# Performance work log

Measured on AMD Instinct MI355X. Metric: run time of the kernel, lower is better.

Reference implementation:

```python
import jax, jax.numpy as jnp
import numpy as np

QMAX = 127.0  # int8 symmetric

def fake_quant(v):
    # symmetric per-tensor int8 quant -> dequant
    s = jnp.maximum(jnp.max(jnp.abs(v)), 1e-8) / QMAX
    return jnp.round(jnp.clip(v / s, -QMAX, QMAX)) * s

def setup_inputs() -> dict:
    key = jax.random.key(0)
    k1, k2, k3 = jax.random.split(key, 3)
    B, C, H, W = 64, 3, 224, 224
    D, P = 768, 8
    x = jax.random.normal(k1, (B, C, H, W), dtype=jnp.float32)
    w = jax.random.normal(k2, (D, C, P, P), dtype=jnp.float32) * 0.02
    b = jax.random.normal(k3, (D,), dtype=jnp.float32) * 0.02
    return {"x": x, "w": w, "b": b}

def reference(x, w, b):
    B, C, H, W = x.shape
    D, _, P, _ = w.shape
    gh, gw = H // P, W // P
    # quantized conv (HMQConv2d): fake-quant activations and weights, then patchify GEMM
    xq = fake_quant(x)
    wq = fake_quant(w)
    # extract non-overlapping PxP patches: [B, C, gh, P, gw, P]
    xp = xq.reshape(B, C, gh, P, gw, P)
    # conv stride=kernel=P  ==  patch matmul: out [B, gh, gw, D]
    out = jnp.einsum('bchpwq,dchq->bhwd', xp.transpose(0, 1, 2, 3, 4, 5), wq,
                     optimize=True) if False else jnp.einsum('bcxpyq,dcpq->bxyd', xp, wq)
    out = out + b
    # flatten(2).transpose(1,2): [B, N, D]
    out = out.reshape(B, gh * gw, D)
    # norm is Identity (norm_layer=None)
    return out
```

## Files before the change

### kernel.cpp

```cpp
#include <hip/hip_runtime.h>
#include <stdint.h>


typedef short bf16x8 __attribute__((ext_vector_type(8)));
using f32x4 = __attribute__((ext_vector_type(4))) float;

static __device__ __forceinline__ uint16_t f2bfbits(float f) {
  uint32_t u = __float_as_uint(f);
  u += 0x7FFFu + ((u >> 16) & 1u);
  return (uint16_t)(u >> 16);
}

static __device__ __forceinline__ uint32_t q2(float a, float b, float inv_s) {
  float qa = rintf(fminf(fmaxf(a * inv_s, -127.0f), 127.0f));
  float qb = rintf(fminf(fmaxf(b * inv_s, -127.0f), 127.0f));
  return (uint32_t)f2bfbits(qa) | ((uint32_t)f2bfbits(qb) << 16);
}

__global__ void absmax_x1_k(const float4* __restrict__ v, int n,
                            float* __restrict__ partials) {
  __shared__ float red[4];
  float m = 0.0f;
  for (int i = blockIdx.x * blockDim.x + threadIdx.x; i < n;
       i += gridDim.x * blockDim.x) {
    float4 u = v[i];
    m = fmaxf(m, fabsf(u.x)); m = fmaxf(m, fabsf(u.y));
    m = fmaxf(m, fabsf(u.z)); m = fmaxf(m, fabsf(u.w));
  }
#pragma unroll
  for (int off = 32; off > 0; off >>= 1) m = fmaxf(m, __shfl_down(m, off, 64));
  if ((threadIdx.x & 63) == 0) red[threadIdx.x >> 6] = m;
  __syncthreads();
  if (threadIdx.x == 0) {
    m = fmaxf(fmaxf(red[0], red[1]), fmaxf(red[2], red[3]));
    partials[blockIdx.x] = m;
  }
}

__global__ void absmax_x2_k(const float* __restrict__ partials,
                            float* __restrict__ s_out) {
  __shared__ float red[16];
  float m = partials[threadIdx.x];
#pragma unroll
  for (int off = 32; off > 0; off >>= 1) m = fmaxf(m, __shfl_down(m, off, 64));
  if ((threadIdx.x & 63) == 0) red[threadIdx.x >> 6] = m;
  __syncthreads();
  if (threadIdx.x == 0) {
#pragma unroll
    for (int i = 1; i < 16; ++i) m = fmaxf(m, red[i]);
    s_out[0] = fmaxf(m, 1e-8f) * (1.0f / 127.0f);
  }
}

__global__ void absmax_w_k(const float4* __restrict__ v, int n,
                           float* __restrict__ s_out) {
  __shared__ float red[16];
  float m = 0.0f;
  for (int i = threadIdx.x; i < n; i += blockDim.x) {
    float4 u = v[i];
    m = fmaxf(m, fabsf(u.x)); m = fmaxf(m, fabsf(u.y));
    m = fmaxf(m, fabsf(u.z)); m = fmaxf(m, fabsf(u.w));
  }
#pragma unroll
  for (int off = 32; off > 0; off >>= 1) m = fmaxf(m, __shfl_down(m, off, 64));
  if ((threadIdx.x & 63) == 0) red[threadIdx.x >> 6] = m;
  __syncthreads();
  if (threadIdx.x == 0) {
#pragma unroll
    for (int i = 1; i < 16; ++i) m = fmaxf(m, red[i]);
    s_out[0] = fmaxf(m, 1e-8f) * (1.0f / 127.0f);
  }
}

__global__ void quant_w_k(const float4* __restrict__ w, uint2* __restrict__ Wq,
                          const float* __restrict__ slots, int n) {
  int tid = blockIdx.x * blockDim.x + threadIdx.x;
  if (tid >= n) return;
  float inv = 1.0f / slots[1];
  float4 u = w[tid];
  Wq[tid] = make_uint2(q2(u.x, u.y, inv), q2(u.z, u.w, inv));
}

#define BM  128
#define BN  128
#define LDP 72

__global__ __launch_bounds__(256) void gemm_k(
    const float4* __restrict__ x4, const uint16_t* __restrict__ Wq,
    const float* __restrict__ bias, const float* __restrict__ slots,
    float* __restrict__ out) {
  __shared__ uint16_t As[BM * LDP];
  __shared__ uint16_t Ws[BN * LDP];

  const int m0   = blockIdx.y * BM;
  const int n0   = blockIdx.x * BN;
  const int tid  = threadIdx.x;
  const int lane = tid & 63;
  const int wid  = tid >> 6;
  const int wm   = wid >> 1;
  const int wn   = wid & 1;
  const int r0   = tid >> 3;
  const int c8   = tid & 7;
  const int lm   = lane & 15;
  const int lq   = lane >> 4;

  const float sx = slots[0];
  const float sw = slots[1];
  const float inv_sx = 1.0f / sx;

  int xbase[4];
#pragma unroll
  for (int i = 0; i < 4; ++i) {
    int m  = m0 + r0 + i * 32;
    int b  = m / 784;
    int rr = m - b * 784;
    int gx = rr / 28;
    int gy = rr - gx * 28;
    xbase[i] = (b * 672 + gx * 8 + c8) * 56 + gy * 2;
  }

  f32x4 acc[4][4] = {};

  for (int kc = 0; kc < 3; ++kc) {
#pragma unroll
    for (int i = 0; i < 4; ++i) {
      int row = r0 + i * 32;
      float4 a0 = x4[xbase[i] + kc * 12544];
      float4 a1 = x4[xbase[i] + kc * 12544 + 1];
      uint4 q;
      q.x = q2(a0.x, a0.y, inv_sx);
      q.y = q2(a0.z, a0.w, inv_sx);
      q.z = q2(a1.x, a1.y, inv_sx);
      q.w = q2(a1.z, a1.w, inv_sx);
      *(uint4*)(&As[row * LDP + c8 * 8]) = q;
      uint4 vb = *(const uint4*)(Wq + (size_t)(n0 + row) * 192 + kc * 64 + c8 * 8);
      *(uint4*)(&Ws[row * LDP + c8 * 8]) = vb;
    }
    __syncthreads();

#pragma unroll
    for (int kk = 0; kk < 2; ++kk) {
      const int colk = kk * 32 + lq * 8;
      bf16x8 af[4], bfr[4];
#pragma unroll
      for (int t = 0; t < 4; ++t) {
        af[t]  = *(const bf16x8*)(&As[(wm * 64 + t * 16 + lm) * LDP + colk]);
        bfr[t] = *(const bf16x8*)(&Ws[(wn * 64 + t * 16 + lm) * LDP + colk]);
      }
#pragma unroll
      for (int tm = 0; tm < 4; ++tm)
#pragma unroll
        for (int tn = 0; tn < 4; ++tn)
          acc[tm][tn] = __builtin_amdgcn_mfma_f32_16x16x32_bf16(
              af[tm], bfr[tn], acc[tm][tn], 0, 0, 0);
    }
    __syncthreads();
  }

  const float scale = sx * sw;
#pragma unroll
  for (int tn = 0; tn < 4; ++tn) {
    int col = n0 + wn * 64 + tn * 16 + lm;
    float bv = bias[col];
#pragma unroll
    for (int tm = 0; tm < 4; ++tm) {
      int rbase = m0 + wm * 64 + tm * 16 + lq * 4;
#pragma unroll
      for (int r = 0; r < 4; ++r) {
        out[(size_t)(rbase + r) * 768 + col] = acc[tm][tn][r] * scale + bv;
      }
    }
  }
}


extern "C" void kernel_launch(void* const* d_in, const int* in_sizes, int n_in,
                              void* d_out, int out_size, void* d_ws, size_t ws_size,
                              hipStream_t stream) {
  const float4* x = (const float4*)d_in[0];
  const float4* w = (const float4*)d_in[1];
  const float* bias = (const float*)d_in[2];
  float* out = (float*)d_out;

  char* ws = (char*)d_ws;
  float* slots    = (float*)ws;
  float* partials = (float*)(ws + 256);
  uint16_t* Wq    = (uint16_t*)(ws + 8192);

  const int nx4 = 9633792 / 4;
  const int nw4 = 147456 / 4;

  absmax_x1_k<<<1024, 256, 0, stream>>>(x, nx4, partials);
  absmax_x2_k<<<1, 1024, 0, stream>>>(partials, slots + 0);
  absmax_w_k<<<1, 1024, 0, stream>>>(w, nw4, slots + 1);
  quant_w_k<<<144, 256, 0, stream>>>(w, (uint2*)Wq, slots, nw4);
  gemm_k<<<dim3(6, 392), 256, 0, stream>>>(x, Wq, bias, slots, out);
}
```

Before: 243.2 us.

## Drop LDS staging and quantize fragments directly from global in GEMM

Merges the x and w absmax reductions into one launch with a shared finalize kernel, and removes the separate weight-quantization kernel. The GEMM now has each wave load its own MFMA A and B fragments straight from global memory and quantize them in registers. This removes the LDS tiles and `__syncthreads` barriers, and cuts the launch count from five to three. In exchange, A and B fragments are loaded and quantized redundantly across waves, and the weights are re-quantized in every block, which leans on L1/L2 caching.

```diff
diff --git a/kernel.cpp b/kernel.cpp
--- a/kernel.cpp
+++ b/kernel.cpp
@@ -10,22 +10,40 @@
   u += 0x7FFFu + ((u >> 16) & 1u);
   return (uint16_t)(u >> 16);
 }
-
 static __device__ __forceinline__ uint32_t q2(float a, float b, float inv_s) {
   float qa = rintf(fminf(fmaxf(a * inv_s, -127.0f), 127.0f));
   float qb = rintf(fminf(fmaxf(b * inv_s, -127.0f), 127.0f));
   return (uint32_t)f2bfbits(qa) | ((uint32_t)f2bfbits(qb) << 16);
 }
+static __device__ __forceinline__ bf16x8 quant_frag(const float4* p, float inv_s) {
+  float4 a0 = p[0], a1 = p[1];
+  uint4 q;
+  q.x = q2(a0.x, a0.y, inv_s);
+  q.y = q2(a0.z, a0.w, inv_s);
+  q.z = q2(a1.x, a1.y, inv_s);
+  q.w = q2(a1.z, a1.w, inv_s);
+  return __builtin_bit_cast(bf16x8, q);
+}
 
-__global__ void absmax_x1_k(const float4* __restrict__ v, int n,
-                            float* __restrict__ partials) {
+#define NBX 1024
+#define NBW 64
+__global__ void absmax_k(const float4* __restrict__ x, int nx4,
+                         const float4* __restrict__ w, int nw4,
+                         float* __restrict__ partials) {
   __shared__ float red[4];
   float m = 0.0f;
-  for (int i = blockIdx.x * blockDim.x + threadIdx.x; i < n;
-       i += gridDim.x * blockDim.x) {
-    float4 u = v[i];
-    m = fmaxf(m, fabsf(u.x)); m = fmaxf(m, fabsf(u.y));
-    m = fmaxf(m, fabsf(u.z)); m = fmaxf(m, fabsf(u.w));
+  if (blockIdx.x < NBX) {
+    for (int i = blockIdx.x * 256 + threadIdx.x; i < nx4; i += NBX * 256) {
+      float4 u = x[i];
+      m = fmaxf(m, fabsf(u.x)); m = fmaxf(m, fabsf(u.y));
+      m = fmaxf(m, fabsf(u.z)); m = fmaxf(m, fabsf(u.w));
+    }
+  } else {
+    for (int i = (blockIdx.x - NBX) * 256 + threadIdx.x; i < nw4; i += NBW * 256) {
+      float4 u = w[i];
+      m = fmaxf(m, fabsf(u.x)); m = fmaxf(m, fabsf(u.y));
+      m = fmaxf(m, fabsf(u.z)); m = fmaxf(m, fabsf(u.w));
+    }
   }
 #pragma unroll
   for (int off = 32; off > 0; off >>= 1) m = fmaxf(m, __shfl_down(m, off, 64));
@@ -37,124 +55,83 @@
   }
 }
 
-__global__ void absmax_x2_k(const float* __restrict__ partials,
-                            float* __restrict__ s_out) {
+__global__ void finalize_k(const float* __restrict__ partials,
+                           float* __restrict__ slots) {
   __shared__ float red[16];
-  float m = partials[threadIdx.x];
+  int tid = threadIdx.x;
+  float m = partials[tid];
 #pragma unroll
   for (int off = 32; off > 0; off >>= 1) m = fmaxf(m, __shfl_down(m, off, 64));
-  if ((threadIdx.x & 63) == 0) red[threadIdx.x >> 6] = m;
+  if ((tid & 63) == 0) red[tid >> 6] = m;
   __syncthreads();
-  if (threadIdx.x == 0) {
+  if (tid == 0) {
 #pragma unroll
     for (int i = 1; i < 16; ++i) m = fmaxf(m, red[i]);
-    s_out[0] = fmaxf(m, 1e-8f) * (1.0f / 127.0f);
+    slots[0] = fmaxf(m, 1e-8f) * (1.0f / 127.0f);
+  }
+  if (tid >= 64 && tid < 128) {
+    float mw = partials[NBX + (tid - 64)];
+#pragma unroll
+    for (int off = 32; off > 0; off >>= 1) mw = fmaxf(mw, __shfl_down(mw, off, 64));
+    if (tid == 64) slots[1] = fmaxf(mw, 1e-8f) * (1.0f / 127.0f);
   }
 }
 
-__global__ void absmax_w_k(const float4* __restrict__ v, int n,
-                           float* __restrict__ s_out) {
-  __shared__ float red[16];
-  float m = 0.0f;
-  for (int i = threadIdx.x; i < n; i += blockDim.x) {
-    float4 u = v[i];
-    m = fmaxf(m, fabsf(u.x)); m = fmaxf(m, fabsf(u.y));
-    m = fmaxf(m, fabsf(u.z)); m = fmaxf(m, fabsf(u.w));
-  }
-#pragma unroll
-  for (int off = 32; off > 0; off >>= 1) m = fmaxf(m, __shfl_down(m, off, 64));
-  if ((threadIdx.x & 63) == 0) red[threadIdx.x >> 6] = m;
-  __syncthreads();
-  if (threadIdx.x == 0) {
-#pragma unroll
-    for (int i = 1; i < 16; ++i) m = fmaxf(m, red[i]);
-    s_out[0] = fmaxf(m, 1e-8f) * (1.0f / 127.0f);
-  }
-}
-
-__global__ void quant_w_k(const float4* __restrict__ w, uint2* __restrict__ Wq,
-                          const float* __restrict__ slots, int n) {
-  int tid = blockIdx.x * blockDim.x + threadIdx.x;
-  if (tid >= n) return;
-  float inv = 1.0f / slots[1];
-  float4 u = w[tid];
-  Wq[tid] = make_uint2(q2(u.x, u.y, inv), q2(u.z, u.w, inv));
-}
-
-#define BM  128
-#define BN  128
-#define LDP 72
-
 __global__ __launch_bounds__(256) void gemm_k(
-    const float4* __restrict__ x4, const uint16_t* __restrict__ Wq,
+    const float4* __restrict__ x4, const float4* __restrict__ w4,
     const float* __restrict__ bias, const float* __restrict__ slots,
     float* __restrict__ out) {
-  __shared__ uint16_t As[BM * LDP];
-  __shared__ uint16_t Ws[BN * LDP];
-
-  const int m0   = blockIdx.y * BM;
-  const int n0   = blockIdx.x * BN;
   const int tid  = threadIdx.x;
   const int lane = tid & 63;
   const int wid  = tid >> 6;
   const int wm   = wid >> 1;
   const int wn   = wid & 1;
-  const int r0   = tid >> 3;
-  const int c8   = tid & 7;
   const int lm   = lane & 15;
   const int lq   = lane >> 4;
+  const int m0   = blockIdx.y * 128;
+  const int n0   = blockIdx.x * 128;
 
   const float sx = slots[0];
   const float sw = slots[1];
   const float inv_sx = 1.0f / sx;
+  const float inv_sw = 1.0f / sw;
 
-  int xbase[4];
+  int abase[4];
 #pragma unroll
-  for (int i = 0; i < 4; ++i) {
-    int m  = m0 + r0 + i * 32;
+  for (int tm = 0; tm < 4; ++tm) {
+    int m  = m0 + wm * 64 + tm * 16 + lm;
     int b  = m / 784;
     int rr = m - b * 784;
     int gx = rr / 28;
     int gy = rr - gx * 28;
-    xbase[i] = (b * 672 + gx * 8 + c8) * 56 + gy * 2;
+    abase[tm] = (b * 672 + gx * 8) * 56 + gy * 2;
   }
+  int bbase[4];
+#pragma unroll
+  for (int tn = 0; tn < 4; ++tn)
+    bbase[tn] = (n0 + wn * 64 + tn * 16 + lm) * 48;
 
   f32x4 acc[4][4] = {};
 
-  for (int kc = 0; kc < 3; ++kc) {
 #pragma unroll
-    for (int i = 0; i < 4; ++i) {
-      int row = r0 + i * 32;
-      float4 a0 = x4[xbase[i] + kc * 12544];
-      float4 a1 = x4[xbase[i] + kc * 12544 + 1];
-      uint4 q;
-      q.x = q2(a0.x, a0.y, inv_sx);
-      q.y = q2(a0.z, a0.w, inv_sx);
-      q.z = q2(a1.x, a1.y, inv_sx);
-      q.w = q2(a1.z, a1.w, inv_sx);
-      *(uint4*)(&As[row * LDP + c8 * 8]) = q;
-      uint4 vb = *(const uint4*)(Wq + (size_t)(n0 + row) * 192 + kc * 64 + c8 * 8);
-      *(uint4*)(&Ws[row * LDP + c8 * 8]) = vb;
-    }
-    __syncthreads();
-
+  for (int ks = 0; ks < 6; ++ks) {
+    const int c = ks >> 1;
+    const int p = (ks & 1) * 4 + lq;
+    const int aoff = c * 12544 + p * 56;
+    const int boff = ks * 8 + lq * 2;
+    bf16x8 af[4], bf[4];
 #pragma unroll
-    for (int kk = 0; kk < 2; ++kk) {
-      const int colk = kk * 32 + lq * 8;
-      bf16x8 af[4], bfr[4];
+    for (int tm = 0; tm < 4; ++tm)
+      af[tm] = quant_frag(&x4[abase[tm] + aoff], inv_sx);
 #pragma unroll
-      for (int t = 0; t < 4; ++t) {
-        af[t]  = *(const bf16x8*)(&As[(wm * 64 + t * 16 + lm) * LDP + colk]);
-        bfr[t] = *(const bf16x8*)(&Ws[(wn * 64 + t * 16 + lm) * LDP + colk]);
-      }
+    for (int tn = 0; tn < 4; ++tn)
+      bf[tn] = quant_frag(&w4[bbase[tn] + boff], inv_sw);
 #pragma unroll
-      for (int tm = 0; tm < 4; ++tm)
+    for (int tm = 0; tm < 4; ++tm)
 #pragma unroll
-        for (int tn = 0; tn < 4; ++tn)
-          acc[tm][tn] = __builtin_amdgcn_mfma_f32_16x16x32_bf16(
-              af[tm], bfr[tn], acc[tm][tn], 0, 0, 0);
-    }
-    __syncthreads();
+      for (int tn = 0; tn < 4; ++tn)
+        acc[tm][tn] = __builtin_amdgcn_mfma_f32_16x16x32_bf16(
+            af[tm], bf[tn], acc[tm][tn], 0, 0, 0);
   }
 
   const float scale = sx * sw;
@@ -166,9 +143,8 @@
     for (int tm = 0; tm < 4; ++tm) {
       int rbase = m0 + wm * 64 + tm * 16 + lq * 4;
 #pragma unroll
-      for (int r = 0; r < 4; ++r) {
+      for (int r = 0; r < 4; ++r)
         out[(size_t)(rbase + r) * 768 + col] = acc[tm][tn][r] * scale + bv;
-      }
     }
   }
 }
@@ -185,14 +161,11 @@
   char* ws = (char*)d_ws;
   float* slots    = (float*)ws;
   float* partials = (float*)(ws + 256);
-  uint16_t* Wq    = (uint16_t*)(ws + 8192);
 
   const int nx4 = 9633792 / 4;
   const int nw4 = 147456 / 4;
 
-  absmax_x1_k<<<1024, 256, 0, stream>>>(x, nx4, partials);
-  absmax_x2_k<<<1, 1024, 0, stream>>>(partials, slots + 0);
-  absmax_w_k<<<1, 1024, 0, stream>>>(w, nw4, slots + 1);
-  quant_w_k<<<144, 256, 0, stream>>>(w, (uint2*)Wq, slots, nw4);
-  gemm_k<<<dim3(6, 392), 256, 0, stream>>>(x, Wq, bias, slots, out);
+  absmax_k<<<NBX + NBW, 256, 0, stream>>>(x, nx4, w, nw4, partials);
+  finalize_k<<<1, 1024, 0, stream>>>(partials, slots);
+  gemm_k<<<dim3(6, 392), 256, 0, stream>>>(x, w, bias, slots, out);
 }
```

Measured after the change: 250.4 us. 2.9% more time.
